# Kernel optimization log

Measured on AMD Instinct MI355X. Metric: run time of the kernel, lower is better.

## Reference

```python
import jax, jax.numpy as jnp
import numpy as np
from jax import lax

N, E, F_NODE, F_EDGE, H, L = 100000, 3200000, 5, 2, 32, 18


def setup_inputs() -> dict:
    key = jax.random.key(0)
    ks = jax.random.split(key, 20)
    s = 0.1
    return {
        "x": jax.random.normal(ks[0], (N, F_NODE), dtype=jnp.float32),
        "edge_attr": jax.random.uniform(ks[1], (E, F_EDGE), dtype=jnp.float32),
        "edge_index": jax.random.randint(ks[2], (2, E), 0, N, dtype=jnp.int32),
        "Wn": jax.random.normal(ks[3], (F_NODE, H), dtype=jnp.float32) * s,
        "bn": jnp.zeros((H,), jnp.float32),
        "We": jax.random.normal(ks[4], (F_EDGE, H), dtype=jnp.float32) * s,
        "be": jnp.zeros((H,), jnp.float32),
        "ln_w": jax.random.normal(ks[5], (L, H, H), dtype=jnp.float32) * s,
        "ln_b": jnp.zeros((L, H), jnp.float32),
        "le_w": jax.random.normal(ks[6], (L, H, H), dtype=jnp.float32) * s,
        "le_b": jnp.zeros((L, H), jnp.float32),
        "lu_w": jax.random.normal(ks[7], (L, 2 * H, H), dtype=jnp.float32) * s,
        "lu_b": jnp.zeros((L, H), jnp.float32),
        "c1_w": jax.random.normal(ks[8], (H, H), dtype=jnp.float32) * s,
        "c1_b": jnp.zeros((H,), jnp.float32),
        "c2_w": jax.random.normal(ks[9], (H, 1), dtype=jnp.float32) * s,
        "c2_b": jnp.zeros((1,), jnp.float32),
    }


def reference(x, edge_attr, edge_index, Wn, bn, We, be,
              ln_w, ln_b, le_w, le_b, lu_w, lu_b, c1_w, c1_b, c2_w, c2_b):
    src, dst = edge_index[0], edge_index[1]
    n = x.shape[0]
    h = x @ Wn + bn                       # [N, H] node encoder
    ea = edge_attr @ We + be              # [E, H] edge encoder (shared by all layers)

    def layer(h, p):
        lnw, lnb, lew, leb, luw, lub = p
        ee = ea @ lew + leb               # [E, H] per-layer edge embedding
        xj = h[src]                       # gather source node states [E, H]
        msg = xj * (1.0 - ee) + ee * (xj @ lnw + lnb)
        agg = jax.ops.segment_sum(msg, dst, num_segments=n)  # scatter-add [N, H]
        out = jnp.concatenate([h, agg], axis=1) @ luw + lub
        return jax.nn.relu(out), None

    h, _ = lax.scan(layer, h, (ln_w, ln_b, le_w, le_b, lu_w, lu_b))
    logits = jax.nn.relu(h @ c1_w + c1_b) @ c2_w + c2_b   # classifier (dropout off at eval)
    return jax.nn.sigmoid(logits).squeeze(-1)             # [N]
```

## Files before the change

### kernel.cpp

```cpp
#include <hip/hip_runtime.h>
#include <hip/hip_bf16.h>
#include <hip/hip_fp8.h>
#include <math.h>

#define H 32
#define SCB 1024
#define S 6

__device__ __forceinline__ unsigned f2bf(float f) {
  unsigned u = __float_as_uint(f);
  return (u + 0x7fffu + ((u >> 16) & 1u)) >> 16;
}
__device__ __forceinline__ float bflo(unsigned p) { return __uint_as_float(p << 16); }
__device__ __forceinline__ float bfhi(unsigned p) { return __uint_as_float(p & 0xffff0000u); }

__device__ __forceinline__ unsigned f2q(float f) {
  __hip_fp8_e4m3 q(f);
  return (unsigned)q.__x;
}
__device__ __forceinline__ float q2f(unsigned b) {
  unsigned s = (b >> 7) & 1u, e = (b >> 3) & 15u, m = b & 7u;
  float vn = __uint_as_float((s << 31) | ((e + 120u) << 23) | (m << 20));
  float vs = __uint_as_float((s << 31) | 0x3f800000u) * ((float)(int)m * (1.0f / 512.0f));
  return (e == 0u) ? vs : vn;
}

template <bool HI>
__device__ __forceinline__ void cvt2(unsigned dw, float& x, float& u) {
#if __has_builtin(__builtin_amdgcn_cvt_pk_f32_fp8)
  typedef float f32x2 __attribute__((ext_vector_type(2)));
  f32x2 v = __builtin_amdgcn_cvt_pk_f32_fp8((int)dw, HI);
  x = v[0]; u = v[1];
#else
  unsigned b = HI ? (dw >> 16) : dw;
  x = q2f(b & 255u); u = q2f((b >> 8) & 255u);
#endif
}

__device__ __forceinline__ unsigned pack4(float x0, float u0, float x1, float u1) {
  return f2q(x0) | (f2q(u0) << 8) | (f2q(x1) << 16) | (f2q(u1) << 24);
}

__global__ void k_encode(const float* __restrict__ x, const float* __restrict__ Wn,
                         const float* __restrict__ bn, const float* __restrict__ lnw0,
                         const float* __restrict__ lnb0, float* __restrict__ h,
                         unsigned* __restrict__ pk, int n, int fnode) {
  __shared__ float sw[H * H];
  int tid = threadIdx.x;
  for (int i = tid; i < H * H; i += blockDim.x) sw[i] = lnw0[i];
  __syncthreads();
  int gid = blockIdx.x * blockDim.x + tid;
  int node = gid >> 5, c = gid & 31;
  if (node >= n) return;
  float acc = bn[c];
  for (int k = 0; k < fnode; ++k)
    acc = fmaf(x[node * fnode + k], Wn[k * H + c], acc);
  h[node * H + c] = acc;
  float t = lnb0[c];
#pragma unroll
  for (int k = 0; k < H; ++k)
    t = fmaf(__shfl(acc, k, 32), sw[k * H + c], t);
  unsigned w = f2q(acc) | (f2q(t - acc) << 8);
  unsigned dw = w | (__shfl_xor(w, 1, 32) << 16);
  if (!(c & 1)) pk[node * 16 + (c >> 1)] = dw;
}

__global__ void k_fold(const float* __restrict__ We, const float* __restrict__ be,
                       const float* __restrict__ lew, const float* __restrict__ leb,
                       float* __restrict__ W2, float* __restrict__ b2, int L) {
  int gid = blockIdx.x * blockDim.x + threadIdx.x;
  if (gid >= L * H) return;
  int l = gid >> 5, c = gid & 31;
  const float* lw = lew + (size_t)l * H * H;
  float a0 = 0.f, a1 = 0.f, bb = leb[l * H + c];
  for (int j = 0; j < H; ++j) {
    float w = lw[j * H + c];
    a0 = fmaf(We[j], w, a0);
    a1 = fmaf(We[H + j], w, a1);
    bb = fmaf(be[j], w, bb);
  }
  W2[l * 2 * H + c] = a0;
  W2[l * 2 * H + H + c] = a1;
  b2[l * H + c] = bb;
}

__global__ void k_hist(const int* __restrict__ dst, unsigned* __restrict__ cnt, int e) {
  int i = blockIdx.x * blockDim.x + threadIdx.x;
  if (i < e) atomicAdd(&cnt[dst[i]], 1u);
}

__global__ void k_scan1(const unsigned* __restrict__ cnt, unsigned* __restrict__ out,
                        unsigned* __restrict__ bsum, int n) {
  __shared__ unsigned s[SCB];
  int i = blockIdx.x * SCB + threadIdx.x;
  unsigned v = (i < n) ? cnt[i] : 0u;
  s[threadIdx.x] = v;
  __syncthreads();
  for (int off = 1; off < SCB; off <<= 1) {
    unsigned u = (threadIdx.x >= off) ? s[threadIdx.x - off] : 0u;
    __syncthreads();
    s[threadIdx.x] += u;
    __syncthreads();
  }
  if (i < n) out[i] = s[threadIdx.x] - v;
  if (threadIdx.x == SCB - 1) bsum[blockIdx.x] = s[SCB - 1];
}

__global__ void k_scan2(const unsigned* __restrict__ bsum, unsigned* __restrict__ boff,
                        unsigned* __restrict__ total_out, int nb) {
  __shared__ unsigned s[SCB];
  unsigned v = ((int)threadIdx.x < nb) ? bsum[threadIdx.x] : 0u;
  s[threadIdx.x] = v;
  __syncthreads();
  for (int off = 1; off < SCB; off <<= 1) {
    unsigned u = (threadIdx.x >= off) ? s[threadIdx.x - off] : 0u;
    __syncthreads();
    s[threadIdx.x] += u;
    __syncthreads();
  }
  if ((int)threadIdx.x < nb) boff[threadIdx.x] = s[threadIdx.x] - v;
  if (threadIdx.x == SCB - 1) *total_out = s[SCB - 1];
}

__global__ void k_scan3(unsigned* __restrict__ row_ptr, const unsigned* __restrict__ boff,
                        unsigned* __restrict__ fill, int n) {
  int i = blockIdx.x * blockDim.x + threadIdx.x;
  if (i >= n) return;
  unsigned v = row_ptr[i] + boff[i >> 10];
  row_ptr[i] = v;
  fill[i] = v;
}

__global__ void k_scatter(const int* __restrict__ src, const int* __restrict__ dst,
                          const float* __restrict__ ea, unsigned* __restrict__ fill,
                          unsigned long long* __restrict__ recs, int e) {
  int i = blockIdx.x * blockDim.x + threadIdx.x;
  if (i >= e) return;
  int d = dst[i];
  unsigned pos = atomicAdd(&fill[d], 1u);
  float2 a = ((const float2*)ea)[i];
  unsigned long long v = (unsigned long long)(unsigned)src[i] |
                         ((unsigned long long)(f2bf(a.x) | (f2bf(a.y) << 16)) << 32);
  __builtin_nontemporal_store(v, &recs[pos]);
}

__device__ __forceinline__ void edge_acc(float (&acc)[8], uint4 pv, unsigned attr, float v,
                                         const float (&w0v)[8], const float (&w1v)[8],
                                         const float (&bbv)[8]) {
  float a0 = bflo(attr), a1 = bfhi(attr);
  unsigned dws[4] = {pv.x, pv.y, pv.z, pv.w};
#pragma unroll
  for (int d = 0; d < 4; ++d) {
    float x0, u0, x1, u1;
    cvt2<false>(dws[d], x0, u0);
    cvt2<true>(dws[d], x1, u1);
    float e0 = fmaf(a0, w0v[2 * d], fmaf(a1, w1v[2 * d], bbv[2 * d]));
    float e1 = fmaf(a0, w0v[2 * d + 1], fmaf(a1, w1v[2 * d + 1], bbv[2 * d + 1]));
    acc[2 * d]     = fmaf(v, fmaf(e0, u0, x0), acc[2 * d]);
    acc[2 * d + 1] = fmaf(v, fmaf(e1, u1, x1), acc[2 * d + 1]);
  }
}

__global__ void __launch_bounds__(256) k_gather(
    const unsigned* __restrict__ pk, const unsigned* __restrict__ row_ptr,
    const unsigned long long* __restrict__ recs, const float* __restrict__ W2l,
    const float* __restrict__ b2l, float* __restrict__ agg, int n, int e) {
  int tid = threadIdx.x;
  int lane = tid & 63;
  int wv = blockIdx.x * 4 + (tid >> 6);
  int n0 = wv * S;
  if (n0 >= n) return;
  int sub = lane & 3;
  unsigned eoff = (unsigned)(lane >> 2);
  float w0v[8], w1v[8], bbv[8];
#pragma unroll
  for (int j = 0; j < 8; ++j) {
    int ch = sub * 8 + j;
    w0v[j] = W2l[ch]; w1v[j] = W2l[H + ch]; bbv[j] = b2l[ch];
  }
  unsigned rp[S + 1];
#pragma unroll
  for (int i = 0; i <= S; ++i) {
    int idx = n0 + i;
    rp[i] = row_ptr[idx < n ? idx : n];
  }
  unsigned b0[S], b1[S], rr[S];
  unsigned R = 0;
#pragma unroll
  for (int s = 0; s < S; ++s) {
    b0[s] = rp[s]; b1[s] = rp[s + 1];
    rr[s] = (b1[s] - b0[s] + 15u) >> 4;
    R = rr[s] > R ? rr[s] : R;
  }
  float acc[S][8] = {};
  const uint4* pk4 = (const uint4*)pk;
  unsigned emax = (unsigned)(e - 1);
  unsigned long long cur[S], nxt[S];
#pragma unroll
  for (int s = 0; s < S; ++s) {
    unsigned ix = b0[s] + eoff;
    unsigned cl = (ix < b1[s]) ? ix : b0[s];
    cl = cl < emax ? cl : emax;
    cur[s] = __builtin_nontemporal_load(&recs[cl]);
  }
  for (unsigned r = 0; r < R; ++r) {
    uint4 pv[S];
#pragma unroll
    for (int s = 0; s < S; ++s)
      if (r < rr[s]) pv[s] = pk4[(size_t)(unsigned)cur[s] * 4 + sub];
#pragma unroll
    for (int s = 0; s < S; ++s) {
      nxt[s] = cur[s];
      if (r + 1 < rr[s]) {
        unsigned ix = b0[s] + (r + 1) * 16u + eoff;
        unsigned cl = (ix < b1[s]) ? ix : b0[s];
        cl = cl < emax ? cl : emax;
        nxt[s] = __builtin_nontemporal_load(&recs[cl]);
      }
    }
    unsigned rb = r << 4;
#pragma unroll
    for (int s = 0; s < S; ++s)
      if (r < rr[s]) {
        float v = (b0[s] + rb + eoff < b1[s]) ? 1.f : 0.f;
        edge_acc(acc[s], pv[s], (unsigned)(cur[s] >> 32), v, w0v, w1v, bbv);
      }
#pragma unroll
    for (int s = 0; s < S; ++s) cur[s] = nxt[s];
  }
#pragma unroll
  for (int s = 0; s < S; ++s)
#pragma unroll
    for (int j = 0; j < 8; ++j) {
      acc[s][j] += __shfl_xor(acc[s][j], 4, 64);
      acc[s][j] += __shfl_xor(acc[s][j], 8, 64);
      acc[s][j] += __shfl_xor(acc[s][j], 16, 64);
      acc[s][j] += __shfl_xor(acc[s][j], 32, 64);
    }
  if (lane < 4) {
#pragma unroll
    for (int s = 0; s < S; ++s) {
      if (n0 + s < n) {
        float4* o = (float4*)&agg[(size_t)(n0 + s) * H + lane * 8];
        o[0] = make_float4(acc[s][0], acc[s][1], acc[s][2], acc[s][3]);
        o[1] = make_float4(acc[s][4], acc[s][5], acc[s][6], acc[s][7]);
      }
    }
  }
}

__global__ void __launch_bounds__(256) k_update(
    const float* __restrict__ h, const float* __restrict__ agg,
    const float* __restrict__ luw, const float* __restrict__ lub,
    const float* __restrict__ lnw, const float* __restrict__ lnb,
    float* __restrict__ hout, unsigned* __restrict__ pkout, int n) {
  int node = blockIdx.x * blockDim.x + threadIdx.x;
  if (node >= n) return;
  float hr[H], ar[H];
  const float4* h4 = (const float4*)(h + (size_t)node * H);
  const float4* a4 = (const float4*)(agg + (size_t)node * H);
#pragma unroll
  for (int q = 0; q < 8; ++q) {
    float4 v = h4[q];
    hr[4 * q] = v.x; hr[4 * q + 1] = v.y; hr[4 * q + 2] = v.z; hr[4 * q + 3] = v.w;
  }
#pragma unroll
  for (int q = 0; q < 8; ++q) {
    float4 v = a4[q];
    ar[4 * q] = v.x; ar[4 * q + 1] = v.y; ar[4 * q + 2] = v.z; ar[4 * q + 3] = v.w;
  }
  float o[H];
#pragma unroll
  for (int c = 0; c < H; ++c) o[c] = lub[c];
#pragma unroll
  for (int k = 0; k < H; ++k)
#pragma unroll
    for (int c = 0; c < H; ++c)
      o[c] = fmaf(hr[k], luw[k * H + c], o[c]);
#pragma unroll
  for (int k = 0; k < H; ++k)
#pragma unroll
    for (int c = 0; c < H; ++c)
      o[c] = fmaf(ar[k], luw[(H + k) * H + c], o[c]);
#pragma unroll
  for (int c = 0; c < H; ++c) o[c] = fmaxf(o[c], 0.f);
  float4* ho = (float4*)(hout + (size_t)node * H);
#pragma unroll
  for (int q = 0; q < 8; ++q)
    ho[q] = make_float4(o[4 * q], o[4 * q + 1], o[4 * q + 2], o[4 * q + 3]);
  if (pkout) {
    float t[H];
#pragma unroll
    for (int c = 0; c < H; ++c) t[c] = lnb[c];
#pragma unroll
    for (int k = 0; k < H; ++k)
#pragma unroll
      for (int c = 0; c < H; ++c)
        t[c] = fmaf(o[k], lnw[k * H + c], t[c]);
    unsigned dws[16];
#pragma unroll
    for (int d = 0; d < 16; ++d)
      dws[d] = pack4(o[2 * d], t[2 * d] - o[2 * d],
                     o[2 * d + 1], t[2 * d + 1] - o[2 * d + 1]);
    uint4* po = (uint4*)(pkout + (size_t)node * 16);
#pragma unroll
    for (int q = 0; q < 4; ++q)
      po[q] = make_uint4(dws[4 * q], dws[4 * q + 1], dws[4 * q + 2], dws[4 * q + 3]);
  }
}

__global__ void k_cls(const float* __restrict__ h, const float* __restrict__ c1w,
                      const float* __restrict__ c1b, const float* __restrict__ c2w,
                      const float* __restrict__ c2b, float* __restrict__ out, int n) {
  __shared__ float sw[H * H];
  int tid = threadIdx.x;
  for (int i = tid; i < H * H; i += blockDim.x) sw[i] = c1w[i];
  __syncthreads();
  int gid = blockIdx.x * blockDim.x + tid;
  int node = gid >> 5, c = gid & 31;
  if (node >= n) return;
  float hv = h[node * H + c];
  float z = c1b[c];
#pragma unroll
  for (int k = 0; k < H; ++k)
    z = fmaf(__shfl(hv, k, 32), sw[k * H + c], z);
  z = fmaxf(z, 0.f);
  float r = z * c2w[c];
#pragma unroll
  for (int m = 16; m >= 1; m >>= 1)
    r += __shfl_xor(r, m, 32);
  if (c == 0) out[node] = 1.f / (1.f + expf(-(r + c2b[0])));
}

extern "C" void kernel_launch(void* const* d_in, const int* in_sizes, int n_in,
                              void* d_out, int out_size, void* d_ws, size_t ws_size,
                              hipStream_t stream) {
  const float* x         = (const float*)d_in[0];
  const float* edge_attr = (const float*)d_in[1];
  const int*   edge_index= (const int*)d_in[2];
  const float* Wn        = (const float*)d_in[3];
  const float* bn        = (const float*)d_in[4];
  const float* We        = (const float*)d_in[5];
  const float* be        = (const float*)d_in[6];
  const float* ln_w      = (const float*)d_in[7];
  const float* ln_b      = (const float*)d_in[8];
  const float* le_w      = (const float*)d_in[9];
  const float* le_b      = (const float*)d_in[10];
  const float* lu_w      = (const float*)d_in[11];
  const float* lu_b      = (const float*)d_in[12];
  const float* c1w       = (const float*)d_in[13];
  const float* c1b       = (const float*)d_in[14];
  const float* c2w       = (const float*)d_in[15];
  const float* c2b       = (const float*)d_in[16];

  const int N_ = in_sizes[0] / 5;
  const int E_ = in_sizes[1] / 2;
  const int L_ = in_sizes[7] / (H * H);
  const int* src = edge_index;
  const int* dst = edge_index + E_;

  char* ws = (char*)d_ws;
  size_t off = 0;
  auto alloc = [&](size_t bytes) -> void* {
    void* p = ws + off;
    off = (off + bytes + 255) & ~(size_t)255;
    return p;
  };
  float*              hA      = (float*)alloc((size_t)N_ * H * 4);
  float*              hB      = (float*)alloc((size_t)N_ * H * 4);
  unsigned*           pkA     = (unsigned*)alloc((size_t)N_ * 16 * 4);
  unsigned*           pkB     = (unsigned*)alloc((size_t)N_ * 16 * 4);
  float*              agg     = (float*)alloc((size_t)N_ * H * 4);
  unsigned*           row_ptr = (unsigned*)alloc((size_t)(N_ + 1) * 4);
  unsigned*           fill    = (unsigned*)alloc((size_t)N_ * 4);
  unsigned long long* recs    = (unsigned long long*)alloc((size_t)E_ * 8);
  float*              W2      = (float*)alloc((size_t)L_ * 2 * H * 4);
  float*              b2      = (float*)alloc((size_t)L_ * H * 4);
  unsigned*           bsum    = (unsigned*)alloc((size_t)SCB * 4);
  unsigned*           boff    = (unsigned*)alloc((size_t)SCB * 4);

  const int tb = 256;
  const int nb = (N_ + SCB - 1) / SCB;
  hipMemsetAsync(fill, 0, (size_t)N_ * 4, stream);
  k_encode<<<(N_ * 32 + tb - 1) / tb, tb, 0, stream>>>(x, Wn, bn, ln_w, ln_b, hA, pkA, N_, 5);
  k_fold<<<(L_ * H + 63) / 64, 64, 0, stream>>>(We, be, le_w, le_b, W2, b2, L_);
  k_hist<<<(E_ + tb - 1) / tb, tb, 0, stream>>>(dst, fill, E_);
  k_scan1<<<nb, SCB, 0, stream>>>(fill, row_ptr, bsum, N_);
  k_scan2<<<1, SCB, 0, stream>>>(bsum, boff, row_ptr + N_, nb);
  k_scan3<<<(N_ + tb - 1) / tb, tb, 0, stream>>>(row_ptr, boff, fill, N_);
  k_scatter<<<(E_ + tb - 1) / tb, tb, 0, stream>>>(src, dst, edge_attr, fill, recs, E_);

  float* hc = hA;  float* hn = hB;
  unsigned* pc = pkA; unsigned* pn = pkB;
  const int gblocks = (N_ + 4 * S - 1) / (4 * S);
  for (int l = 0; l < L_; ++l) {
    bool last = (l == L_ - 1);
    k_gather<<<gblocks, 256, 0, stream>>>(
        pc, row_ptr, recs, W2 + l * 2 * H, b2 + l * H, agg, N_, E_);
    k_update<<<(N_ + tb - 1) / tb, tb, 0, stream>>>(
        hc, agg, lu_w + (size_t)l * 2 * H * H, lu_b + (size_t)l * H,
        last ? nullptr : ln_w + (size_t)(l + 1) * H * H,
        last ? nullptr : ln_b + (size_t)(l + 1) * H,
        hn, last ? nullptr : pn, N_);
    float* tf = hc; hc = hn; hn = tf;
    unsigned* tp = pc; pc = pn; pn = tp;
  }
  k_cls<<<(N_ * 32 + tb - 1) / tb, tb, 0, stream>>>(hc, c1w, c1b, c2w, c2b, (float*)d_out, N_);
}
```

Measured before the change: 2.260 ms.

## Split packed node features into channel halves and gather each half separately

The packed fp8 node table is split into two 16-channel halves stored in separate arrays. The edge gather kernel now runs twice per layer, once per half, so each pass randomly reads from a table half the size, which should fit better in cache. The price is that the edge record stream and row pointers are read twice per layer and there are extra launches. Nodes per wave drop from 6 to 4, and the scatter now uses plain stores instead of nontemporal stores.

```diff
diff --git a/kernel.cpp b/kernel.cpp
--- a/kernel.cpp
+++ b/kernel.cpp
@@ -5,7 +5,7 @@
 
 #define H 32
 #define SCB 1024
-#define S 6
+#define S 4
 
 __device__ __forceinline__ unsigned f2bf(float f) {
   unsigned u = __float_as_uint(f);
@@ -44,7 +44,8 @@
 __global__ void k_encode(const float* __restrict__ x, const float* __restrict__ Wn,
                          const float* __restrict__ bn, const float* __restrict__ lnw0,
                          const float* __restrict__ lnb0, float* __restrict__ h,
-                         unsigned* __restrict__ pk, int n, int fnode) {
+                         unsigned* __restrict__ pk0, unsigned* __restrict__ pk1,
+                         int n, int fnode) {
   __shared__ float sw[H * H];
   int tid = threadIdx.x;
   for (int i = tid; i < H * H; i += blockDim.x) sw[i] = lnw0[i];
@@ -62,7 +63,10 @@
     t = fmaf(__shfl(acc, k, 32), sw[k * H + c], t);
   unsigned w = f2q(acc) | (f2q(t - acc) << 8);
   unsigned dw = w | (__shfl_xor(w, 1, 32) << 16);
-  if (!(c & 1)) pk[node * 16 + (c >> 1)] = dw;
+  if (!(c & 1)) {
+    unsigned* ph = (c < 16) ? pk0 : pk1;
+    ph[node * 8 + ((c & 15) >> 1)] = dw;
+  }
 }
 
 __global__ void k_fold(const float* __restrict__ We, const float* __restrict__ be,
@@ -139,18 +143,17 @@
   int d = dst[i];
   unsigned pos = atomicAdd(&fill[d], 1u);
   float2 a = ((const float2*)ea)[i];
-  unsigned long long v = (unsigned long long)(unsigned)src[i] |
-                         ((unsigned long long)(f2bf(a.x) | (f2bf(a.y) << 16)) << 32);
-  __builtin_nontemporal_store(v, &recs[pos]);
-}
-
-__device__ __forceinline__ void edge_acc(float (&acc)[8], uint4 pv, unsigned attr, float v,
-                                         const float (&w0v)[8], const float (&w1v)[8],
-                                         const float (&bbv)[8]) {
+  recs[pos] = (unsigned long long)(unsigned)src[i] |
+              ((unsigned long long)(f2bf(a.x) | (f2bf(a.y) << 16)) << 32);
+}
+
+__device__ __forceinline__ void edge_acc4(float (&acc)[4], uint2 pv, unsigned attr, float v,
+                                          const float (&w0v)[4], const float (&w1v)[4],
+                                          const float (&bbv)[4]) {
   float a0 = bflo(attr), a1 = bfhi(attr);
-  unsigned dws[4] = {pv.x, pv.y, pv.z, pv.w};
-#pragma unroll
-  for (int d = 0; d < 4; ++d) {
+  unsigned dws[2] = {pv.x, pv.y};
+#pragma unroll
+  for (int d = 0; d < 2; ++d) {
     float x0, u0, x1, u1;
     cvt2<false>(dws[d], x0, u0);
     cvt2<true>(dws[d], x1, u1);
@@ -162,9 +165,9 @@
 }
 
 __global__ void __launch_bounds__(256) k_gather(
-    const unsigned* __restrict__ pk, const unsigned* __restrict__ row_ptr,
+    const unsigned* __restrict__ pkh, const unsigned* __restrict__ row_ptr,
     const unsigned long long* __restrict__ recs, const float* __restrict__ W2l,
-    const float* __restrict__ b2l, float* __restrict__ agg, int n, int e) {
+    const float* __restrict__ b2l, int co, float* __restrict__ agg, int n, int e) {
   int tid = threadIdx.x;
   int lane = tid & 63;
   int wv = blockIdx.x * 4 + (tid >> 6);
@@ -172,10 +175,10 @@
   if (n0 >= n) return;
   int sub = lane & 3;
   unsigned eoff = (unsigned)(lane >> 2);
-  float w0v[8], w1v[8], bbv[8];
-#pragma unroll
-  for (int j = 0; j < 8; ++j) {
-    int ch = sub * 8 + j;
+  float w0v[4], w1v[4], bbv[4];
+#pragma unroll
+  for (int j = 0; j < 4; ++j) {
+    int ch = co + sub * 4 + j;
     w0v[j] = W2l[ch]; w1v[j] = W2l[H + ch]; bbv[j] = b2l[ch];
   }
   unsigned rp[S + 1];
@@ -192,8 +195,8 @@
     rr[s] = (b1[s] - b0[s] + 15u) >> 4;
     R = rr[s] > R ? rr[s] : R;
   }
-  float acc[S][8] = {};
-  const uint4* pk4 = (const uint4*)pk;
+  float acc[S][4] = {};
+  const uint2* pk2 = (const uint2*)pkh;
   unsigned emax = (unsigned)(e - 1);
   unsigned long long cur[S], nxt[S];
 #pragma unroll
@@ -204,10 +207,10 @@
     cur[s] = __builtin_nontemporal_load(&recs[cl]);
   }
   for (unsigned r = 0; r < R; ++r) {
-    uint4 pv[S];
+    uint2 pv[S];
 #pragma unroll
     for (int s = 0; s < S; ++s)
-      if (r < rr[s]) pv[s] = pk4[(size_t)(unsigned)cur[s] * 4 + sub];
+      if (r < rr[s]) pv[s] = pk2[(size_t)(unsigned)cur[s] * 4 + sub];
 #pragma unroll
     for (int s = 0; s < S; ++s) {
       nxt[s] = cur[s];
@@ -223,7 +226,7 @@
     for (int s = 0; s < S; ++s)
       if (r < rr[s]) {
         float v = (b0[s] + rb + eoff < b1[s]) ? 1.f : 0.f;
-        edge_acc(acc[s], pv[s], (unsigned)(cur[s] >> 32), v, w0v, w1v, bbv);
+        edge_acc4(acc[s], pv[s], (unsigned)(cur[s] >> 32), v, w0v, w1v, bbv);
       }
 #pragma unroll
     for (int s = 0; s < S; ++s) cur[s] = nxt[s];
@@ -231,7 +234,7 @@
 #pragma unroll
   for (int s = 0; s < S; ++s)
 #pragma unroll
-    for (int j = 0; j < 8; ++j) {
+    for (int j = 0; j < 4; ++j) {
       acc[s][j] += __shfl_xor(acc[s][j], 4, 64);
       acc[s][j] += __shfl_xor(acc[s][j], 8, 64);
       acc[s][j] += __shfl_xor(acc[s][j], 16, 64);
@@ -241,9 +244,8 @@
 #pragma unroll
     for (int s = 0; s < S; ++s) {
       if (n0 + s < n) {
-        float4* o = (float4*)&agg[(size_t)(n0 + s) * H + lane * 8];
+        float4* o = (float4*)&agg[(size_t)(n0 + s) * H + co + lane * 4];
         o[0] = make_float4(acc[s][0], acc[s][1], acc[s][2], acc[s][3]);
-        o[1] = make_float4(acc[s][4], acc[s][5], acc[s][6], acc[s][7]);
       }
     }
   }
@@ -253,7 +255,8 @@
     const float* __restrict__ h, const float* __restrict__ agg,
     const float* __restrict__ luw, const float* __restrict__ lub,
     const float* __restrict__ lnw, const float* __restrict__ lnb,
-    float* __restrict__ hout, unsigned* __restrict__ pkout, int n) {
+    float* __restrict__ hout, unsigned* __restrict__ pk0,
+    unsigned* __restrict__ pk1, int n) {
   int node = blockIdx.x * blockDim.x + threadIdx.x;
   if (node >= n) return;
   float hr[H], ar[H];
@@ -288,7 +291,7 @@
 #pragma unroll
   for (int q = 0; q < 8; ++q)
     ho[q] = make_float4(o[4 * q], o[4 * q + 1], o[4 * q + 2], o[4 * q + 3]);
-  if (pkout) {
+  if (pk0) {
     float t[H];
 #pragma unroll
     for (int c = 0; c < H; ++c) t[c] = lnb[c];
@@ -302,10 +305,12 @@
     for (int d = 0; d < 16; ++d)
       dws[d] = pack4(o[2 * d], t[2 * d] - o[2 * d],
                      o[2 * d + 1], t[2 * d + 1] - o[2 * d + 1]);
-    uint4* po = (uint4*)(pkout + (size_t)node * 16);
-#pragma unroll
-    for (int q = 0; q < 4; ++q)
-      po[q] = make_uint4(dws[4 * q], dws[4 * q + 1], dws[4 * q + 2], dws[4 * q + 3]);
+    uint4* p0 = (uint4*)(pk0 + (size_t)node * 8);
+    p0[0] = make_uint4(dws[0], dws[1], dws[2], dws[3]);
+    p0[1] = make_uint4(dws[4], dws[5], dws[6], dws[7]);
+    uint4* p1 = (uint4*)(pk1 + (size_t)node * 8);
+    p1[0] = make_uint4(dws[8], dws[9], dws[10], dws[11]);
+    p1[1] = make_uint4(dws[12], dws[13], dws[14], dws[15]);
   }
 }
 
@@ -368,8 +373,10 @@
   };
   float*              hA      = (float*)alloc((size_t)N_ * H * 4);
   float*              hB      = (float*)alloc((size_t)N_ * H * 4);
-  unsigned*           pkA     = (unsigned*)alloc((size_t)N_ * 16 * 4);
-  unsigned*           pkB     = (unsigned*)alloc((size_t)N_ * 16 * 4);
+  unsigned*           pkA0    = (unsigned*)alloc((size_t)N_ * 8 * 4);
+  unsigned*           pkA1    = (unsigned*)alloc((size_t)N_ * 8 * 4);
+  unsigned*           pkB0    = (unsigned*)alloc((size_t)N_ * 8 * 4);
+  unsigned*           pkB1    = (unsigned*)alloc((size_t)N_ * 8 * 4);
   float*              agg     = (float*)alloc((size_t)N_ * H * 4);
   unsigned*           row_ptr = (unsigned*)alloc((size_t)(N_ + 1) * 4);
   unsigned*           fill    = (unsigned*)alloc((size_t)N_ * 4);
@@ -382,7 +389,7 @@
   const int tb = 256;
   const int nb = (N_ + SCB - 1) / SCB;
   hipMemsetAsync(fill, 0, (size_t)N_ * 4, stream);
-  k_encode<<<(N_ * 32 + tb - 1) / tb, tb, 0, stream>>>(x, Wn, bn, ln_w, ln_b, hA, pkA, N_, 5);
+  k_encode<<<(N_ * 32 + tb - 1) / tb, tb, 0, stream>>>(x, Wn, bn, ln_w, ln_b, hA, pkA0, pkA1, N_, 5);
   k_fold<<<(L_ * H + 63) / 64, 64, 0, stream>>>(We, be, le_w, le_b, W2, b2, L_);
   k_hist<<<(E_ + tb - 1) / tb, tb, 0, stream>>>(dst, fill, E_);
   k_scan1<<<nb, SCB, 0, stream>>>(fill, row_ptr, bsum, N_);
@@ -391,19 +398,23 @@
   k_scatter<<<(E_ + tb - 1) / tb, tb, 0, stream>>>(src, dst, edge_attr, fill, recs, E_);
 
   float* hc = hA;  float* hn = hB;
-  unsigned* pc = pkA; unsigned* pn = pkB;
+  unsigned* pc0 = pkA0; unsigned* pc1 = pkA1;
+  unsigned* pn0 = pkB0; unsigned* pn1 = pkB1;
   const int gblocks = (N_ + 4 * S - 1) / (4 * S);
   for (int l = 0; l < L_; ++l) {
     bool last = (l == L_ - 1);
-    k_gather<<<gblocks, 256, 0, stream>>>(
-        pc, row_ptr, recs, W2 + l * 2 * H, b2 + l * H, agg, N_, E_);
+    const float* w2l = W2 + l * 2 * H;
+    const float* b2l = b2 + l * H;
+    k_gather<<<gblocks, 256, 0, stream>>>(pc0, row_ptr, recs, w2l, b2l, 0, agg, N_, E_);
+    k_gather<<<gblocks, 256, 0, stream>>>(pc1, row_ptr, recs, w2l, b2l, 16, agg, N_, E_);
     k_update<<<(N_ + tb - 1) / tb, tb, 0, stream>>>(
         hc, agg, lu_w + (size_t)l * 2 * H * H, lu_b + (size_t)l * H,
         last ? nullptr : ln_w + (size_t)(l + 1) * H * H,
         last ? nullptr : ln_b + (size_t)(l + 1) * H,
-        hn, last ? nullptr : pn, N_);
+        hn, last ? nullptr : pn0, last ? nullptr : pn1, N_);
     float* tf = hc; hc = hn; hn = tf;
-    unsigned* tp = pc; pc = pn; pn = tp;
+    unsigned* t0 = pc0; pc0 = pn0; pn0 = t0;
+    unsigned* t1 = pc1; pc1 = pn1; pn1 = t1;
   }
   k_cls<<<(N_ * 32 + tb - 1) / tb, tb, 0, stream>>>(hc, c1w, c1b, c2w, c2b, (float*)d_out, N_);
 }
```

Result: slower. 2.525 ms (+11.7%).
